# Optimization experiments

Measured on AMD Instinct MI355X. Metric: run time of the kernel, lower is better.

The kernel has to match this reference:

```python
import jax
jax.config.update("jax_enable_x64", True)
import jax.numpy as jnp
import numpy as np

B, T, C, H = 4, 4096, 120, 64  # batch, seq, n_embed, head_size


def setup_inputs() -> dict:
    key = jax.random.key(0)
    kx, kk, kq, kv = jax.random.split(key, 4)
    x = jax.random.normal(kx, (B, T, C), dtype=jnp.float32)
    s = 1.0 / np.sqrt(C)  # ~nn.Linear init scale
    Wk = jax.random.normal(kk, (C, H), dtype=jnp.float32) * s
    Wq = jax.random.normal(kq, (C, H), dtype=jnp.float32) * s
    Wv = jax.random.normal(kv, (C, H), dtype=jnp.float32) * s
    return {"x": x, "Wk": Wk, "Wq": Wq, "Wv": Wv}


def reference(x, Wk, Wq, Wv):
    # Original module runs entirely in float64 (.double()).
    x = x.astype(jnp.float64)
    Wk = Wk.astype(jnp.float64)
    Wq = Wq.astype(jnp.float64)
    Wv = Wv.astype(jnp.float64)
    k = jnp.einsum("btc,ch->bth", x, Wk)
    q = jnp.einsum("btc,ch->bth", x, Wq)
    v = jnp.einsum("btc,ch->bth", x, Wv)
    scale = x.shape[-1] ** (-0.5)  # NOTE: scales by n_embed (C), not head_size
    wei = jnp.einsum("bth,bsh->bts", q, k) * scale  # [B, T, T]
    wei = jax.nn.softmax(wei, axis=-1)
    # dropout(p=0.01) is identity in eval mode
    out = jnp.einsum("bts,bsh->bth", wei, v)  # [B, T, H]
    return out
```

## Files before the change

kernel.cpp:

```cpp
#include <hip/hip_runtime.h>

typedef __attribute__((ext_vector_type(2))) float f32x2;
typedef __attribute__((ext_vector_type(4))) float f32x4;
typedef __attribute__((ext_vector_type(8))) short s16x8;
typedef __attribute__((ext_vector_type(2))) unsigned int u32x2;
typedef __attribute__((ext_vector_type(4))) unsigned int u32x4;

#define BN 4
#define TN 4096
#define CN 120
#define HN 64

__device__ __forceinline__ unsigned short f2bf(float f) {
  unsigned int u = __float_as_uint(f);
  unsigned int r = (u + 0x7fffu + ((u >> 16) & 1u)) >> 16;
  return (unsigned short)r;
}
__device__ __forceinline__ float bf2f(unsigned short h) {
  return __uint_as_float((unsigned int)h << 16);
}
__device__ __forceinline__ float fast_exp2(float x) {
#if __has_builtin(__builtin_amdgcn_exp2f)
  return __builtin_amdgcn_exp2f(x);
#else
  return exp2f(x);
#endif
}


__global__ __launch_bounds__(256, 3) void proj_kernel(
    const float* __restrict__ x, const float* __restrict__ Wk,
    const float* __restrict__ Wq, const float* __restrict__ Wv,
    unsigned short* __restrict__ Kf, unsigned short* __restrict__ Qg,
    unsigned short* __restrict__ Vf) {
  __shared__ struct {
    unsigned short xh[64][136];
    unsigned short xl[64][136];
    unsigned short vt[64][72];
  } sm;
  const int tid = threadIdx.x;
  const int mat = blockIdx.x >> 8;
  const int rb = blockIdx.x & 255;
  const int row0 = rb * 64;
  const int wave = tid >> 6, lane = tid & 63;
  const int l15 = lane & 15, quad = lane >> 4;
  const int b = row0 >> 12, key0 = row0 & (TN - 1);

  const float* Ws = (mat == 0) ? Wk : (mat == 1) ? Wq : Wv;
  const float wsc = (mat == 1) ? 0.13169944f : 1.0f;
  s16x8 wh[4], wl[4];
#pragma unroll
  for (int kc = 0; kc < 4; ++kc) {
#pragma unroll
    for (int j = 0; j < 8; ++j) {
      const int c = kc * 32 + quad * 8 + j;
      const float w = (c < CN) ? Ws[c * HN + wave * 16 + l15] * wsc : 0.f;
      const unsigned short h16 = f2bf(w);
      wh[kc][j] = (short)h16;
      wl[kc][j] = (short)f2bf(w - bf2f(h16));
    }
  }

  for (int n = tid; n < 64 * 30; n += 256) {
    const int row = n / 30, c4 = n - row * 30;
    const f32x4 xv = *(const f32x4*)&x[(size_t)(row0 + row) * CN + c4 * 4];
    u32x2 hp, lp;
#pragma unroll
    for (int e = 0; e < 2; ++e) {
      const unsigned short h0 = f2bf(xv[2 * e]);
      const unsigned short h1 = f2bf(xv[2 * e + 1]);
      hp[e] = (unsigned int)h0 | ((unsigned int)h1 << 16);
      lp[e] = (unsigned int)f2bf(xv[2 * e] - bf2f(h0)) |
              ((unsigned int)f2bf(xv[2 * e + 1] - bf2f(h1)) << 16);
    }
    *(u32x2*)&sm.xh[row][c4 * 4] = hp;
    *(u32x2*)&sm.xl[row][c4 * 4] = lp;
  }
  if (tid < 64) {
    const u32x4 z = {0u, 0u, 0u, 0u};
    *(u32x4*)&sm.xh[tid][120] = z;
    *(u32x4*)&sm.xl[tid][120] = z;
  }
  __syncthreads();

  f32x4 acc[4];
#pragma unroll
  for (int mt = 0; mt < 4; ++mt) acc[mt] = 0.f;
#pragma unroll
  for (int mt = 0; mt < 4; ++mt) {
#pragma unroll
    for (int kc = 0; kc < 4; ++kc) {
      const s16x8 ah = *(const s16x8*)&sm.xh[mt * 16 + l15][kc * 32 + quad * 8];
      const s16x8 al = *(const s16x8*)&sm.xl[mt * 16 + l15][kc * 32 + quad * 8];
      acc[mt] = __builtin_amdgcn_mfma_f32_16x16x32_bf16(al, wh[kc], acc[mt], 0, 0, 0);
      acc[mt] = __builtin_amdgcn_mfma_f32_16x16x32_bf16(ah, wl[kc], acc[mt], 0, 0, 0);
      acc[mt] = __builtin_amdgcn_mfma_f32_16x16x32_bf16(ah, wh[kc], acc[mt], 0, 0, 0);
    }
  }

  if (mat < 2) {
#pragma unroll
    for (int mt = 0; mt < 4; ++mt)
#pragma unroll
      for (int r = 0; r < 4; ++r)
        sm.vt[mt * 16 + quad * 4 + r][wave * 16 + l15] = f2bf(acc[mt][r]);
    __syncthreads();
    if (mat == 1) {
      const int row = tid >> 2, seg = tid & 3;
      const u32x4 d0 = *(const u32x4*)&sm.vt[row][seg * 16];
      const u32x4 d1 = *(const u32x4*)&sm.vt[row][seg * 16 + 8];
      unsigned short* qp = &Qg[(size_t)(row0 + row) * HN + seg * 16];
      *(u32x4*)qp = d0;
      *(u32x4*)(qp + 8) = d1;
    } else {
#pragma unroll
      for (int i = 0; i < 2; ++i) {
        const int c = tid + i * 256;
        const int ktl = c >> 7, ch = (c >> 6) & 1, L = c & 63;
        const u32x4 d =
            *(const u32x4*)&sm.vt[ktl * 16 + (L & 15)][(L >> 4) * 8 + ch * 32];
        *(u32x4*)((unsigned char*)Kf +
                  (((size_t)b * 256 + (key0 >> 4) + ktl) * 128 + ch * 64 + L) *
                      16) = d;
      }
    }
  } else {
#pragma unroll
    for (int mt = 0; mt < 4; ++mt)
#pragma unroll
      for (int r = 0; r < 4; ++r)
        sm.vt[wave * 16 + l15][mt * 16 + quad * 4 + r] = f2bf(acc[mt][r]);
    __syncthreads();
#pragma unroll
    for (int i = 0; i < 2; ++i) {
      const int c = tid + i * 256;
      const int kbl = c >> 8, ht = (c >> 6) & 3, L = c & 63;
      const u32x4 d =
          *(const u32x4*)&sm.vt[ht * 16 + (L & 15)][kbl * 32 + (L >> 4) * 8];
      *(u32x4*)((unsigned char*)Vf +
                (((size_t)b * 128 + (key0 >> 5) + kbl) * 4 + ht) * 1024 +
                L * 16) = d;
    }
  }
}

__global__ __launch_bounds__(512, 4) void attn_kernel(
    const unsigned short* __restrict__ Qg, const unsigned short* __restrict__ Kf,
    const unsigned short* __restrict__ Vf, float* __restrict__ out) {
  __shared__ union {
    unsigned short p[8][2][16][72];
    struct { float ob[8][64][17]; float lb[8][16]; } m;
  } sm;
  const int bid = blockIdx.x;
  const int xslot = bid & 7;
  const int b = xslot >> 1;
  const int qt5 = (bid >> 3) | ((xslot & 1) << 6);
  const int qbase = qt5 * 32;
  const int tid = threadIdx.x;
  const int wave = tid >> 6, lane = tid & 63;
  const int l15 = lane & 15, quad = lane >> 4;

  s16x8 qf[2][2];
#pragma unroll
  for (int qt = 0; qt < 2; ++qt) {
    const unsigned short* qrow =
        Qg + (size_t)(b * TN + qbase + qt * 16 + l15) * HN + quad * 8;
    qf[qt][0] = *(const s16x8*)qrow;
    qf[qt][1] = *(const s16x8*)(qrow + 32);
  }

  const unsigned char* Kfb = (const unsigned char*)Kf + (size_t)b * 524288;
  const unsigned char* Vfb = (const unsigned char*)Vf + (size_t)b * 524288;
  char* pw[2];
#pragma unroll
  for (int qt = 0; qt < 2; ++qt)
    pw[qt] = (char*)&sm.p[wave][qt][0][0] + l15 * 144;

  f32x4 o[2][4];
#pragma unroll
  for (int qt = 0; qt < 2; ++qt)
#pragma unroll
    for (int t = 0; t < 4; ++t) o[qt][t] = 0.f;
  float lacc[2] = {0.f, 0.f};

  const int kb0 = wave * 512;
#pragma unroll 1
  for (int it = 0; it < 8; ++it) {
    const int kb = kb0 + it * 64;
#pragma unroll
    for (int t = 0; t < 4; ++t) {
      const unsigned char* ktp =
          Kfb + (size_t)((kb >> 4) + t) * 2048 + lane * 16;
      const s16x8 a0 = *(const s16x8*)ktp;
      const s16x8 a1 = *(const s16x8*)(ktp + 1024);
      f32x4 s0 = 0.f, s1 = 0.f;
      s0 = __builtin_amdgcn_mfma_f32_16x16x32_bf16(a0, qf[0][0], s0, 0, 0, 0);
      s0 = __builtin_amdgcn_mfma_f32_16x16x32_bf16(a1, qf[0][1], s0, 0, 0, 0);
      s1 = __builtin_amdgcn_mfma_f32_16x16x32_bf16(a0, qf[1][0], s1, 0, 0, 0);
      s1 = __builtin_amdgcn_mfma_f32_16x16x32_bf16(a1, qf[1][1], s1, 0, 0, 0);
#pragma unroll
      for (int qt = 0; qt < 2; ++qt) {
        const f32x4 s = qt ? s1 : s0;
        unsigned int u0 = __float_as_uint(fast_exp2(fminf(s[0], 80.f)));
        unsigned int u1 = __float_as_uint(fast_exp2(fminf(s[1], 80.f)));
        unsigned int u2 = __float_as_uint(fast_exp2(fminf(s[2], 80.f)));
        unsigned int u3 = __float_as_uint(fast_exp2(fminf(s[3], 80.f)));
        u0 &= 0xffff0000u; u1 &= 0xffff0000u;
        u2 &= 0xffff0000u; u3 &= 0xffff0000u;
        lacc[qt] += (__uint_as_float(u0) + __uint_as_float(u1)) +
                    (__uint_as_float(u2) + __uint_as_float(u3));
        u32x2 w;
        w.x = (u0 >> 16) | u1;
        w.y = (u2 >> 16) | u3;
        *(u32x2*)(pw[qt] + t * 32 + quad * 8) = w;
      }
    }
#pragma unroll 1
    for (int kc = 0; kc < 2; ++kc) {
      const s16x8 pb0 = *(const s16x8*)(pw[0] + quad * 16 + kc * 64);
      const s16x8 pb1 = *(const s16x8*)(pw[1] + quad * 16 + kc * 64);
#pragma unroll
      for (int ht = 0; ht < 4; ++ht) {
        const unsigned char* vtp =
            Vfb + (size_t)((kb >> 5) + kc) * 4096 + ht * 1024 + lane * 16;
        const s16x8 va = *(const s16x8*)vtp;
        o[0][ht] = __builtin_amdgcn_mfma_f32_16x16x32_bf16(va, pb0, o[0][ht], 0, 0, 0);
        o[1][ht] = __builtin_amdgcn_mfma_f32_16x16x32_bf16(va, pb1, o[1][ht], 0, 0, 0);
      }
    }
  }
#pragma unroll
  for (int qt = 0; qt < 2; ++qt) {
    lacc[qt] += __shfl_xor(lacc[qt], 16, 64);
    lacc[qt] += __shfl_xor(lacc[qt], 32, 64);
  }
  __syncthreads();
#pragma unroll
  for (int qt = 0; qt < 2; ++qt) {
    if (lane < 16) sm.m.lb[wave][l15] = lacc[qt];
#pragma unroll
    for (int ht = 0; ht < 4; ++ht)
#pragma unroll
      for (int r = 0; r < 4; ++r)
        sm.m.ob[wave][ht * 16 + quad * 4 + r][l15] = o[qt][ht][r];
    __syncthreads();
    const int h = tid & 63;
    const int wq = tid >> 6;
#pragma unroll
    for (int i = 0; i < 2; ++i) {
      const int qq = (i << 3) | wq;
      float ssum = 0.f, ll = 0.f;
#pragma unroll
      for (int w = 0; w < 8; ++w) {
        ssum += sm.m.ob[w][h][qq];
        ll += sm.m.lb[w][qq];
      }
      out[(size_t)(b * TN + qbase + qt * 16 + qq) * HN + h] = ssum / ll;
    }
    __syncthreads();
  }
}

extern "C" void kernel_launch(void* const* d_in, const int* in_sizes, int n_in,
                              void* d_out, int out_size, void* d_ws,
                              size_t ws_size, hipStream_t stream) {
  const float* x = (const float*)d_in[0];
  const float* Wk = (const float*)d_in[1];
  const float* Wq = (const float*)d_in[2];
  const float* Wv = (const float*)d_in[3];
  unsigned short* Kf = (unsigned short*)d_ws;
  unsigned short* Qg = Kf + (size_t)BN * TN * HN;
  unsigned short* Vf = Qg + (size_t)BN * TN * HN;
  float* out = (float*)d_out;
  proj_kernel<<<768, 256, 0, stream>>>(x, Wk, Wq, Wv, Kf, Qg, Vf);
  attn_kernel<<<BN * TN / 32, 512, 0, stream>>>(Qg, Kf, Vf, out);
}
```

Measured before the change: 99.19 us.

## Double query tile per block to 64 rows and prefetch K fragments

Each attention block now handles 64 query rows (four 16-row tiles) instead of 32, so every K and V fragment loaded from global memory feeds twice as many MFMAs. The grid halves to 256 blocks, shared memory becomes dynamic (72 KB), and launch bounds drop to 2 blocks per CU. K fragments for the next iteration are prefetched into registers before the PV stage, and the bf16 packing uses a byte-permute instruction. The cost is higher register and LDS use, lower occupancy, and fewer blocks to spread across CUs.

```diff
diff --git a/kernel.cpp b/kernel.cpp
--- a/kernel.cpp
+++ b/kernel.cpp
@@ -144,25 +144,22 @@
   }
 }
 
-__global__ __launch_bounds__(512, 4) void attn_kernel(
+__global__ __launch_bounds__(512, 2) void attn_kernel(
     const unsigned short* __restrict__ Qg, const unsigned short* __restrict__ Kf,
     const unsigned short* __restrict__ Vf, float* __restrict__ out) {
-  __shared__ union {
-    unsigned short p[8][2][16][72];
-    struct { float ob[8][64][17]; float lb[8][16]; } m;
-  } sm;
+  extern __shared__ unsigned char smraw[];
   const int bid = blockIdx.x;
   const int xslot = bid & 7;
   const int b = xslot >> 1;
-  const int qt5 = (bid >> 3) | ((xslot & 1) << 6);
-  const int qbase = qt5 * 32;
+  const int qt6 = (bid >> 3) | ((xslot & 1) << 5);
+  const int qbase = qt6 * 64;
   const int tid = threadIdx.x;
   const int wave = tid >> 6, lane = tid & 63;
   const int l15 = lane & 15, quad = lane >> 4;
 
-  s16x8 qf[2][2];
-#pragma unroll
-  for (int qt = 0; qt < 2; ++qt) {
+  s16x8 qf[4][2];
+#pragma unroll
+  for (int qt = 0; qt < 4; ++qt) {
     const unsigned short* qrow =
         Qg + (size_t)(b * TN + qbase + qt * 16 + l15) * HN + quad * 8;
     qf[qt][0] = *(const s16x8*)qrow;
@@ -171,54 +168,75 @@
 
   const unsigned char* Kfb = (const unsigned char*)Kf + (size_t)b * 524288;
   const unsigned char* Vfb = (const unsigned char*)Vf + (size_t)b * 524288;
-  char* pw[2];
-#pragma unroll
-  for (int qt = 0; qt < 2; ++qt)
-    pw[qt] = (char*)&sm.p[wave][qt][0][0] + l15 * 144;
-
-  f32x4 o[2][4];
-#pragma unroll
-  for (int qt = 0; qt < 2; ++qt)
+  char* pw[4];
+#pragma unroll
+  for (int qt = 0; qt < 4; ++qt)
+    pw[qt] = (char*)smraw + (wave * 4 + qt) * 2304 + l15 * 144;
+
+  f32x4 o[4][4];
+#pragma unroll
+  for (int qt = 0; qt < 4; ++qt)
 #pragma unroll
     for (int t = 0; t < 4; ++t) o[qt][t] = 0.f;
-  float lacc[2] = {0.f, 0.f};
+  float lacc[4] = {0.f, 0.f, 0.f, 0.f};
 
   const int kb0 = wave * 512;
+
+  s16x8 ka[4][2];
+#pragma unroll
+  for (int t = 0; t < 4; ++t) {
+    const unsigned char* ktp = Kfb + (size_t)((kb0 >> 4) + t) * 2048 + lane * 16;
+    ka[t][0] = *(const s16x8*)ktp;
+    ka[t][1] = *(const s16x8*)(ktp + 1024);
+  }
+
 #pragma unroll 1
   for (int it = 0; it < 8; ++it) {
     const int kb = kb0 + it * 64;
 #pragma unroll
     for (int t = 0; t < 4; ++t) {
-      const unsigned char* ktp =
-          Kfb + (size_t)((kb >> 4) + t) * 2048 + lane * 16;
-      const s16x8 a0 = *(const s16x8*)ktp;
-      const s16x8 a1 = *(const s16x8*)(ktp + 1024);
-      f32x4 s0 = 0.f, s1 = 0.f;
-      s0 = __builtin_amdgcn_mfma_f32_16x16x32_bf16(a0, qf[0][0], s0, 0, 0, 0);
-      s0 = __builtin_amdgcn_mfma_f32_16x16x32_bf16(a1, qf[0][1], s0, 0, 0, 0);
-      s1 = __builtin_amdgcn_mfma_f32_16x16x32_bf16(a0, qf[1][0], s1, 0, 0, 0);
-      s1 = __builtin_amdgcn_mfma_f32_16x16x32_bf16(a1, qf[1][1], s1, 0, 0, 0);
-#pragma unroll
-      for (int qt = 0; qt < 2; ++qt) {
-        const f32x4 s = qt ? s1 : s0;
+      f32x4 s0 = 0.f, s1 = 0.f, s2 = 0.f, s3 = 0.f;
+      s0 = __builtin_amdgcn_mfma_f32_16x16x32_bf16(ka[t][0], qf[0][0], s0, 0, 0, 0);
+      s0 = __builtin_amdgcn_mfma_f32_16x16x32_bf16(ka[t][1], qf[0][1], s0, 0, 0, 0);
+      s1 = __builtin_amdgcn_mfma_f32_16x16x32_bf16(ka[t][0], qf[1][0], s1, 0, 0, 0);
+      s1 = __builtin_amdgcn_mfma_f32_16x16x32_bf16(ka[t][1], qf[1][1], s1, 0, 0, 0);
+      s2 = __builtin_amdgcn_mfma_f32_16x16x32_bf16(ka[t][0], qf[2][0], s2, 0, 0, 0);
+      s2 = __builtin_amdgcn_mfma_f32_16x16x32_bf16(ka[t][1], qf[2][1], s2, 0, 0, 0);
+      s3 = __builtin_amdgcn_mfma_f32_16x16x32_bf16(ka[t][0], qf[3][0], s3, 0, 0, 0);
+      s3 = __builtin_amdgcn_mfma_f32_16x16x32_bf16(ka[t][1], qf[3][1], s3, 0, 0, 0);
+#pragma unroll
+      for (int qt = 0; qt < 4; ++qt) {
+        const f32x4 s = (qt == 0) ? s0 : (qt == 1) ? s1 : (qt == 2) ? s2 : s3;
         unsigned int u0 = __float_as_uint(fast_exp2(fminf(s[0], 80.f)));
         unsigned int u1 = __float_as_uint(fast_exp2(fminf(s[1], 80.f)));
         unsigned int u2 = __float_as_uint(fast_exp2(fminf(s[2], 80.f)));
         unsigned int u3 = __float_as_uint(fast_exp2(fminf(s[3], 80.f)));
-        u0 &= 0xffff0000u; u1 &= 0xffff0000u;
-        u2 &= 0xffff0000u; u3 &= 0xffff0000u;
-        lacc[qt] += (__uint_as_float(u0) + __uint_as_float(u1)) +
-                    (__uint_as_float(u2) + __uint_as_float(u3));
+        const unsigned int m0 = u0 & 0xffff0000u, m1 = u1 & 0xffff0000u;
+        const unsigned int m2 = u2 & 0xffff0000u, m3 = u3 & 0xffff0000u;
+        lacc[qt] += (__uint_as_float(m0) + __uint_as_float(m1)) +
+                    (__uint_as_float(m2) + __uint_as_float(m3));
         u32x2 w;
-        w.x = (u0 >> 16) | u1;
-        w.y = (u2 >> 16) | u3;
+        w.x = __builtin_amdgcn_perm(u1, u0, 0x07060302u);
+        w.y = __builtin_amdgcn_perm(u3, u2, 0x07060302u);
         *(u32x2*)(pw[qt] + t * 32 + quad * 8) = w;
       }
     }
-#pragma unroll 1
+    if (it < 7) {
+      const int kbn = kb + 64;
+#pragma unroll
+      for (int t = 0; t < 4; ++t) {
+        const unsigned char* ktp =
+            Kfb + (size_t)((kbn >> 4) + t) * 2048 + lane * 16;
+        ka[t][0] = *(const s16x8*)ktp;
+        ka[t][1] = *(const s16x8*)(ktp + 1024);
+      }
+    }
+#pragma unroll
     for (int kc = 0; kc < 2; ++kc) {
       const s16x8 pb0 = *(const s16x8*)(pw[0] + quad * 16 + kc * 64);
       const s16x8 pb1 = *(const s16x8*)(pw[1] + quad * 16 + kc * 64);
+      const s16x8 pb2 = *(const s16x8*)(pw[2] + quad * 16 + kc * 64);
+      const s16x8 pb3 = *(const s16x8*)(pw[3] + quad * 16 + kc * 64);
 #pragma unroll
       for (int ht = 0; ht < 4; ++ht) {
         const unsigned char* vtp =
@@ -226,23 +244,27 @@
         const s16x8 va = *(const s16x8*)vtp;
         o[0][ht] = __builtin_amdgcn_mfma_f32_16x16x32_bf16(va, pb0, o[0][ht], 0, 0, 0);
         o[1][ht] = __builtin_amdgcn_mfma_f32_16x16x32_bf16(va, pb1, o[1][ht], 0, 0, 0);
-      }
-    }
-  }
-#pragma unroll
-  for (int qt = 0; qt < 2; ++qt) {
+        o[2][ht] = __builtin_amdgcn_mfma_f32_16x16x32_bf16(va, pb2, o[2][ht], 0, 0, 0);
+        o[3][ht] = __builtin_amdgcn_mfma_f32_16x16x32_bf16(va, pb3, o[3][ht], 0, 0, 0);
+      }
+    }
+  }
+#pragma unroll
+  for (int qt = 0; qt < 4; ++qt) {
     lacc[qt] += __shfl_xor(lacc[qt], 16, 64);
     lacc[qt] += __shfl_xor(lacc[qt], 32, 64);
   }
   __syncthreads();
-#pragma unroll
-  for (int qt = 0; qt < 2; ++qt) {
-    if (lane < 16) sm.m.lb[wave][l15] = lacc[qt];
+  float* ob = (float*)smraw;
+  float* lb = (float*)(smraw + 8 * 64 * 17 * 4);
+#pragma unroll
+  for (int qt = 0; qt < 4; ++qt) {
+    if (lane < 16) lb[wave * 16 + l15] = lacc[qt];
 #pragma unroll
     for (int ht = 0; ht < 4; ++ht)
 #pragma unroll
       for (int r = 0; r < 4; ++r)
-        sm.m.ob[wave][ht * 16 + quad * 4 + r][l15] = o[qt][ht][r];
+        ob[(wave * 64 + ht * 16 + quad * 4 + r) * 17 + l15] = o[qt][ht][r];
     __syncthreads();
     const int h = tid & 63;
     const int wq = tid >> 6;
@@ -252,8 +274,8 @@
       float ssum = 0.f, ll = 0.f;
 #pragma unroll
       for (int w = 0; w < 8; ++w) {
-        ssum += sm.m.ob[w][h][qq];
-        ll += sm.m.lb[w][qq];
+        ssum += ob[(w * 64 + h) * 17 + qq];
+        ll += lb[w * 16 + qq];
       }
       out[(size_t)(b * TN + qbase + qt * 16 + qq) * HN + h] = ssum / ll;
     }
@@ -272,6 +294,13 @@
   unsigned short* Qg = Kf + (size_t)BN * TN * HN;
   unsigned short* Vf = Qg + (size_t)BN * TN * HN;
   float* out = (float*)d_out;
+  static bool smset = false;
+  if (!smset) {
+    (void)hipFuncSetAttribute((const void*)attn_kernel,
+                              hipFuncAttributeMaxDynamicSharedMemorySize,
+                              73728);
+    smset = true;
+  }
   proj_kernel<<<768, 256, 0, stream>>>(x, Wk, Wq, Wv, Kf, Qg, Vf);
-  attn_kernel<<<BN * TN / 32, 512, 0, stream>>>(Qg, Kf, Vf, out);
-}
+  attn_kernel<<<BN * TN / 64, 512, 73728, stream>>>(Qg, Kf, Vf, out);
+}
```

Measured after the change: 104.9 us. 5.7% more time.

## Software-pipeline K/V fragment loads and raise MFMA wave priority

Applied to the files above, without the earlier changes.

Prefetches the K fragments for the next 64-key block into registers during the current iteration, and issues the V fragment loads early, overlapping them with the QK MFMAs and exp work. It also wraps MFMA groups in s_setprio to favour matrix issue across waves, and replaces the shift/or bf16 packing with a single v_perm byte permute. The cost is higher register pressure from the double-buffered K/V fragments, which could reduce occupancy.

```diff
diff --git a/kernel.cpp b/kernel.cpp
--- a/kernel.cpp
+++ b/kernel.cpp
@@ -169,8 +169,10 @@
     qf[qt][1] = *(const s16x8*)(qrow + 32);
   }
 
-  const unsigned char* Kfb = (const unsigned char*)Kf + (size_t)b * 524288;
-  const unsigned char* Vfb = (const unsigned char*)Vf + (size_t)b * 524288;
+  const unsigned char* Kfl =
+      (const unsigned char*)Kf + (size_t)b * 524288 + lane * 16;
+  const unsigned char* Vfl =
+      (const unsigned char*)Vf + (size_t)b * 524288 + lane * 16;
   char* pw[2];
 #pragma unroll
   for (int qt = 0; qt < 2; ++qt)
@@ -184,20 +186,37 @@
   float lacc[2] = {0.f, 0.f};
 
   const int kb0 = wave * 512;
+
+  s16x8 ka[4][2];
+#pragma unroll
+  for (int t = 0; t < 4; ++t) {
+    const unsigned char* kt = Kfl + (size_t)((kb0 >> 4) + t) * 2048;
+    ka[t][0] = *(const s16x8*)kt;
+    ka[t][1] = *(const s16x8*)(kt + 1024);
+  }
+
 #pragma unroll 1
   for (int it = 0; it < 8; ++it) {
     const int kb = kb0 + it * 64;
+    const unsigned char* vbase = Vfl + (size_t)(kb >> 5) * 4096;
+    s16x8 va0[4], va1[4];
+#pragma unroll
+    for (int ht = 0; ht < 4; ++ht)
+      va0[ht] = *(const s16x8*)(vbase + ht * 1024);
 #pragma unroll
     for (int t = 0; t < 4; ++t) {
-      const unsigned char* ktp =
-          Kfb + (size_t)((kb >> 4) + t) * 2048 + lane * 16;
-      const s16x8 a0 = *(const s16x8*)ktp;
-      const s16x8 a1 = *(const s16x8*)(ktp + 1024);
+      if (t == 2) {
+#pragma unroll
+        for (int ht = 0; ht < 4; ++ht)
+          va1[ht] = *(const s16x8*)(vbase + 4096 + ht * 1024);
+      }
       f32x4 s0 = 0.f, s1 = 0.f;
-      s0 = __builtin_amdgcn_mfma_f32_16x16x32_bf16(a0, qf[0][0], s0, 0, 0, 0);
-      s0 = __builtin_amdgcn_mfma_f32_16x16x32_bf16(a1, qf[0][1], s0, 0, 0, 0);
-      s1 = __builtin_amdgcn_mfma_f32_16x16x32_bf16(a0, qf[1][0], s1, 0, 0, 0);
-      s1 = __builtin_amdgcn_mfma_f32_16x16x32_bf16(a1, qf[1][1], s1, 0, 0, 0);
+      __builtin_amdgcn_s_setprio(1);
+      s0 = __builtin_amdgcn_mfma_f32_16x16x32_bf16(ka[t][0], qf[0][0], s0, 0, 0, 0);
+      s0 = __builtin_amdgcn_mfma_f32_16x16x32_bf16(ka[t][1], qf[0][1], s0, 0, 0, 0);
+      s1 = __builtin_amdgcn_mfma_f32_16x16x32_bf16(ka[t][0], qf[1][0], s1, 0, 0, 0);
+      s1 = __builtin_amdgcn_mfma_f32_16x16x32_bf16(ka[t][1], qf[1][1], s1, 0, 0, 0);
+      __builtin_amdgcn_s_setprio(0);
 #pragma unroll
       for (int qt = 0; qt < 2; ++qt) {
         const f32x4 s = qt ? s1 : s0;
@@ -205,28 +224,46 @@
         unsigned int u1 = __float_as_uint(fast_exp2(fminf(s[1], 80.f)));
         unsigned int u2 = __float_as_uint(fast_exp2(fminf(s[2], 80.f)));
         unsigned int u3 = __float_as_uint(fast_exp2(fminf(s[3], 80.f)));
-        u0 &= 0xffff0000u; u1 &= 0xffff0000u;
-        u2 &= 0xffff0000u; u3 &= 0xffff0000u;
-        lacc[qt] += (__uint_as_float(u0) + __uint_as_float(u1)) +
-                    (__uint_as_float(u2) + __uint_as_float(u3));
+        const unsigned int m0 = u0 & 0xffff0000u, m1 = u1 & 0xffff0000u;
+        const unsigned int m2 = u2 & 0xffff0000u, m3 = u3 & 0xffff0000u;
+        lacc[qt] += (__uint_as_float(m0) + __uint_as_float(m1)) +
+                    (__uint_as_float(m2) + __uint_as_float(m3));
         u32x2 w;
-        w.x = (u0 >> 16) | u1;
-        w.y = (u2 >> 16) | u3;
+        w.x = __builtin_amdgcn_perm(u1, u0, 0x07060302u);
+        w.y = __builtin_amdgcn_perm(u3, u2, 0x07060302u);
         *(u32x2*)(pw[qt] + t * 32 + quad * 8) = w;
       }
     }
-#pragma unroll 1
-    for (int kc = 0; kc < 2; ++kc) {
-      const s16x8 pb0 = *(const s16x8*)(pw[0] + quad * 16 + kc * 64);
-      const s16x8 pb1 = *(const s16x8*)(pw[1] + quad * 16 + kc * 64);
+    {
+      const s16x8 pb0 = *(const s16x8*)(pw[0] + quad * 16);
+      const s16x8 pb1 = *(const s16x8*)(pw[1] + quad * 16);
+      __builtin_amdgcn_s_setprio(1);
 #pragma unroll
       for (int ht = 0; ht < 4; ++ht) {
-        const unsigned char* vtp =
-            Vfb + (size_t)((kb >> 5) + kc) * 4096 + ht * 1024 + lane * 16;
-        const s16x8 va = *(const s16x8*)vtp;
-        o[0][ht] = __builtin_amdgcn_mfma_f32_16x16x32_bf16(va, pb0, o[0][ht], 0, 0, 0);
-        o[1][ht] = __builtin_amdgcn_mfma_f32_16x16x32_bf16(va, pb1, o[1][ht], 0, 0, 0);
-      }
+        o[0][ht] = __builtin_amdgcn_mfma_f32_16x16x32_bf16(va0[ht], pb0, o[0][ht], 0, 0, 0);
+        o[1][ht] = __builtin_amdgcn_mfma_f32_16x16x32_bf16(va0[ht], pb1, o[1][ht], 0, 0, 0);
+      }
+      __builtin_amdgcn_s_setprio(0);
+    }
+    if (it < 7) {
+      const int kbn = kb + 64;
+#pragma unroll
+      for (int t = 0; t < 4; ++t) {
+        const unsigned char* kt = Kfl + (size_t)((kbn >> 4) + t) * 2048;
+        ka[t][0] = *(const s16x8*)kt;
+        ka[t][1] = *(const s16x8*)(kt + 1024);
+      }
+    }
+    {
+      const s16x8 pb0 = *(const s16x8*)(pw[0] + quad * 16 + 64);
+      const s16x8 pb1 = *(const s16x8*)(pw[1] + quad * 16 + 64);
+      __builtin_amdgcn_s_setprio(1);
+#pragma unroll
+      for (int ht = 0; ht < 4; ++ht) {
+        o[0][ht] = __builtin_amdgcn_mfma_f32_16x16x32_bf16(va1[ht], pb0, o[0][ht], 0, 0, 0);
+        o[1][ht] = __builtin_amdgcn_mfma_f32_16x16x32_bf16(va1[ht], pb1, o[1][ht], 0, 0, 0);
+      }
+      __builtin_amdgcn_s_setprio(0);
     }
   }
 #pragma unroll
```

New measurement: 154.7 us. +56.0%, slower.
